# Performance work log

Measured on AMD Instinct MI355X. Metric: run time of the kernel, lower is better.

Reference implementation:

```python
import jax, jax.numpy as jnp
import numpy as np

N = 8192
F_IN = 512
H = 512
E = 128
ALPHA = 0.2
NEG = -9e15


def _xavier(key, shape, gain=1.414):
    fan_in, fan_out = shape[0], shape[1]
    bound = gain * np.sqrt(6.0 / (fan_in + fan_out))
    return jax.random.uniform(key, shape, jnp.float32, -bound, bound)


def setup_inputs() -> dict:
    key = jax.random.key(0)
    ks = jax.random.split(key, 9)
    x = jax.random.normal(ks[0], (N, F_IN), jnp.float32)
    u = jax.random.uniform(ks[1], (N, N), jnp.float32)
    adj = jnp.where(u < 0.05, u, 0.0)
    M = jax.random.uniform(ks[2], (N, N), jnp.float32)
    return {
        "x": x, "adj": adj, "M": M,
        "W1": _xavier(ks[3], (F_IN, H)),
        "a_self1": _xavier(ks[4], (H, 1)),
        "a_neigh1": _xavier(ks[5], (H, 1)),
        "W2": _xavier(ks[6], (H, E)),
        "a_self2": _xavier(ks[7], (E, 1)),
        "a_neigh2": _xavier(ks[8], (E, 1)),
    }


def _gat_layer(x, adj, M, W, a_self, a_neigh):
    h = x @ W                                   # (N, out)
    s = h @ a_self                              # (N, 1)
    n = h @ a_neigh                             # (N, 1)
    e = (s + n.T) * M                           # (N, N) broadcast score sum
    e = jnp.where(e > 0, e, ALPHA * e)          # leaky_relu
    masked = jnp.where(adj > 0, e, NEG)
    attn = jax.nn.softmax(masked, axis=1)
    h_prime = attn @ h
    return jax.nn.elu(h_prime)


def reference(x, adj, M, W1, a_self1, a_neigh1, W2, a_self2, a_neigh2):
    h = _gat_layer(x, adj, M, W1, a_self1, a_neigh1)
    h = _gat_layer(h, adj, M, W2, a_self2, a_neigh2)
    z = h / jnp.maximum(jnp.linalg.norm(h, axis=1, keepdims=True), 1e-12)
    A_pred = jax.nn.sigmoid(z @ z.T)
    return (A_pred, z)
```

## Files before the change

kernel.cpp:

```cpp
#include <hip/hip_runtime.h>
#include <math.h>

#define NNODES 8192
#define CAP 1024
#define KSPLIT 4
#define KCHUNK (NNODES / KSPLIT)

typedef __attribute__((ext_vector_type(8))) short bf16x8;
typedef __attribute__((ext_vector_type(4))) float f32x4;
typedef unsigned short ushort_t;

__device__ inline unsigned short f2bf(float x) {
    unsigned u = __builtin_bit_cast(unsigned, x);
    u += 0x7fffu + ((u >> 16) & 1u);
    return (unsigned short)(u >> 16);
}

#define GLOAD_LDS16(g, l)                                                      \
    __builtin_amdgcn_global_load_lds(                                          \
        (const __attribute__((address_space(1))) void*)(g),                    \
        (__attribute__((address_space(3))) void*)(l), 16, 0, 0)

template <int ROWS>
__device__ inline void stage_tile(ushort_t* lds, const ushort_t* g, size_t ld, int tid)
{
#pragma unroll
    for (int c = 0; c < ROWS / 32; ++c) {
        int row = c * 32 + (tid >> 3);
        int lch = (tid & 7) ^ (row & 7);
        GLOAD_LDS16(g + (size_t)row * ld + lch * 8, lds + (size_t)c * 2048 + tid * 8);
    }
}

__device__ inline int swz_off(int row, int kc) {
    return row * 64 + ((kc ^ (row & 7)) * 8);
}

__global__ __launch_bounds__(256) void gemm64(const float* __restrict__ A,
                                              const float* __restrict__ B,
                                              float* __restrict__ C,
                                              int M, int N, int K)
{
    __shared__ float sA[16][68];
    __shared__ float sB[16][68];

    const int tid = threadIdx.x;
    const int tx = tid & 15, ty = tid >> 4;
    const int bm = blockIdx.x * 64, bn = blockIdx.y * 64;

    float acc[4][4] = {};

    for (int k0 = 0; k0 < K; k0 += 16) {
        for (int l = tid; l < 64 * 16; l += 256) {
            int m = l >> 4, k = l & 15;
            sA[k][m] = A[(size_t)(bm + m) * K + k0 + k];
        }
        for (int l = tid; l < 16 * 64; l += 256) {
            int k = l >> 6, n = l & 63;
            sB[k][n] = B[(size_t)(k0 + k) * N + bn + n];
        }
        __syncthreads();
#pragma unroll
        for (int k = 0; k < 16; ++k) {
            float a[4], b[4];
#pragma unroll
            for (int i = 0; i < 4; ++i) a[i] = sA[k][ty * 4 + i];
#pragma unroll
            for (int j = 0; j < 4; ++j) b[j] = sB[k][tx * 4 + j];
#pragma unroll
            for (int i = 0; i < 4; ++i)
#pragma unroll
                for (int j = 0; j < 4; ++j) acc[i][j] += a[i] * b[j];
        }
        __syncthreads();
    }

#pragma unroll
    for (int i = 0; i < 4; ++i) {
        float4 v = make_float4(acc[i][0], acc[i][1], acc[i][2], acc[i][3]);
        *(float4*)&C[(size_t)(bm + ty * 4 + i) * N + bn + tx * 4] = v;
    }
}

template <int D>
__global__ __launch_bounds__(256) void sn_kernel(const float* __restrict__ h,
                                                 const float* __restrict__ a_s,
                                                 const float* __restrict__ a_n,
                                                 float* __restrict__ sv,
                                                 float* __restrict__ nv)
{
    const int row = (blockIdx.x * 256 + threadIdx.x) >> 6;
    const int lane = threadIdx.x & 63;
    if (row >= NNODES) return;
    const float* hr = h + (size_t)row * D;
    float a0 = 0.f, a1 = 0.f;
#pragma unroll
    for (int k = lane; k < D; k += 64) {
        float hv = hr[k];
        a0 += hv * a_s[k];
        a1 += hv * a_n[k];
    }
#pragma unroll
    for (int o = 32; o; o >>= 1) {
        a0 += __shfl_down(a0, o);
        a1 += __shfl_down(a1, o);
    }
    if (lane == 0) { sv[row] = a0; nv[row] = a1; }
}

__global__ __launch_bounds__(256) void build_csr(const float* __restrict__ adj,
                                                 const float* __restrict__ Mm,
                                                 unsigned short* __restrict__ cols,
                                                 float* __restrict__ vals,
                                                 int* __restrict__ nnzs)
{
    __shared__ __align__(16) float sadj[4][4][256];
    __shared__ __align__(16) float smv[4][4][256];
    __shared__ unsigned short lcol[4][CAP];
    __shared__ float lval[4][CAP];

    const int tid = threadIdx.x;
    const int wid = tid >> 6, lane = tid & 63;
    const int row = blockIdx.x * 4 + wid;
    const float* arow = adj + (size_t)row * NNODES;
    const float* mrow = Mm + (size_t)row * NNODES;
    const size_t base = (size_t)row * CAP;
    const unsigned long long below = (1ull << lane) - 1ull;

    float* sa = &sadj[wid][0][0];
    float* sm = &smv[wid][0][0];
    unsigned short* sc = lcol[wid];
    float* svl = lval[wid];

    int off = 0;

#define ISSUE(t)                                                               \
    do {                                                                       \
        int _s = (t) & 3;                                                      \
        GLOAD_LDS16(arow + (t) * 256 + lane * 4, sa + _s * 256 + lane * 4);    \
        GLOAD_LDS16(mrow + (t) * 256 + lane * 4, sm + _s * 256 + lane * 4);    \
    } while (0)

#define PROCESS(t)                                                             \
    do {                                                                       \
        int _s = (t) & 3;                                                      \
        float4 a = *(const float4*)(sa + _s * 256 + lane * 4);                 \
        float4 mv = *(const float4*)(sm + _s * 256 + lane * 4);                \
        _Pragma("unroll")                                                      \
        for (int e = 0; e < 4; ++e) {                                          \
            float ae = (&a.x)[e];                                              \
            unsigned long long mask = __ballot(ae > 0.f);                      \
            if (ae > 0.f) {                                                    \
                int pos = off + __popcll(mask & below);                        \
                if (pos < CAP) {                                               \
                    sc[pos] = (unsigned short)((t) * 256 + lane * 4 + e);      \
                    svl[pos] = (&mv.x)[e];                                     \
                }                                                              \
            }                                                                  \
            off += __popcll(mask);                                             \
        }                                                                      \
    } while (0)

    ISSUE(0); ISSUE(1); ISSUE(2); ISSUE(3);

    for (int t = 0; t < 28; ++t) {
        asm volatile("s_waitcnt vmcnt(6)" ::: "memory");
        __builtin_amdgcn_sched_barrier(0);
        PROCESS(t);
        ISSUE(t + 4);
    }
    asm volatile("s_waitcnt vmcnt(6)" ::: "memory");
    __builtin_amdgcn_sched_barrier(0);
    PROCESS(28);
    asm volatile("s_waitcnt vmcnt(4)" ::: "memory");
    __builtin_amdgcn_sched_barrier(0);
    PROCESS(29);
    asm volatile("s_waitcnt vmcnt(2)" ::: "memory");
    __builtin_amdgcn_sched_barrier(0);
    PROCESS(30);
    asm volatile("s_waitcnt vmcnt(0)" ::: "memory");
    __builtin_amdgcn_sched_barrier(0);
    PROCESS(31);

#undef ISSUE
#undef PROCESS

    const int nnz = min(off, CAP);
    for (int k = lane; k < nnz; k += 64) {
        cols[base + k] = sc[k];
        vals[base + k] = svl[k];
    }
    if (lane == 0) nnzs[row] = off;
}

__global__ __launch_bounds__(256) void softmax_dense(const unsigned short* __restrict__ cols,
                                                     const float* __restrict__ vals,
                                                     const int* __restrict__ nnzs,
                                                     const float* __restrict__ sv,
                                                     const float* __restrict__ nv,
                                                     ushort_t* __restrict__ P)
{
    constexpr int NT = 256;
    __shared__ ushort_t drow[NNODES];
    __shared__ unsigned short scol[CAP];
    __shared__ float sp[CAP];
    __shared__ float reds[4];
    __shared__ float fb;

    const int tid = threadIdx.x;
    const int i = blockIdx.x;
    const int nnz = min(nnzs[i], CAP);
    const float si = sv[i];
    const size_t base = (size_t)i * CAP;

#pragma unroll
    for (int k = 0; k < NNODES / 8 / NT; ++k)
        ((uint4*)drow)[k * NT + tid] = (uint4){0u, 0u, 0u, 0u};

    float lmax = -3.0e38f;
    for (int k = tid; k < nnz; k += NT) {
        unsigned short c = cols[base + k];
        float e = (si + nv[c]) * vals[base + k];
        e = e > 0.f ? e : 0.2f * e;
        scol[k] = c;
        sp[k] = e;
        lmax = fmaxf(lmax, e);
    }
#pragma unroll
    for (int o = 32; o; o >>= 1) lmax = fmaxf(lmax, __shfl_down(lmax, o));
    if ((tid & 63) == 0) reds[tid >> 6] = lmax;
    __syncthreads();
    if (tid == 0) fb = fmaxf(fmaxf(reds[0], reds[1]), fmaxf(reds[2], reds[3]));
    __syncthreads();
    const float m = fb;

    float lsum = 0.f;
    for (int k = tid; k < nnz; k += NT) {
        float p = expf(sp[k] - m);
        sp[k] = p;
        lsum += p;
    }
#pragma unroll
    for (int o = 32; o; o >>= 1) lsum += __shfl_down(lsum, o);
    if ((tid & 63) == 0) reds[tid >> 6] = lsum;
    __syncthreads();
    if (tid == 0) fb = reds[0] + reds[1] + reds[2] + reds[3];
    __syncthreads();
    const float inv = 1.0f / fb;

    for (int k = tid; k < nnz; k += NT)
        drow[scol[k]] = f2bf(sp[k] * inv);
    __syncthreads();

    uint4* dst = (uint4*)(P + (size_t)i * NNODES);
#pragma unroll
    for (int k = 0; k < NNODES / 8 / NT; ++k)
        dst[k * NT + tid] = ((const uint4*)drow)[k * NT + tid];
}

__global__ __launch_bounds__(256) void tcast(const float* __restrict__ in,
                                             ushort_t* __restrict__ out,
                                             int R, int C)
{
    __shared__ ushort_t t[64][66];
    const int bi = blockIdx.x;
    const int bj = blockIdx.y;
    const int c = threadIdx.x & 63, r4 = threadIdx.x >> 6;
#pragma unroll
    for (int i = 0; i < 16; ++i) {
        int r = i * 4 + r4;
        t[r][c] = f2bf(in[(size_t)(bi * 64 + r) * C + bj * 64 + c]);
    }
    __syncthreads();
#pragma unroll
    for (int i = 0; i < 16; ++i) {
        int r = i * 4 + r4;
        out[(size_t)(bj * 64 + r) * R + bi * 64 + c] = t[c][r];
    }
}

__global__ __launch_bounds__(256) void cast_bf(const float* __restrict__ in,
                                               ushort_t* __restrict__ out, int n4)
{
    int i = blockIdx.x * 256 + threadIdx.x;
    if (i >= n4) return;
    float4 v = ((const float4*)in)[i];
    ushort_t o[4] = { f2bf(v.x), f2bf(v.y), f2bf(v.z), f2bf(v.w) };
    *(uint2*)&out[(size_t)i * 4] = *(uint2*)o;
}

template <int ELU>
__global__ __launch_bounds__(256) void gemm_mfma(const ushort_t* __restrict__ A,
                                                 const ushort_t* __restrict__ BT,
                                                 float* __restrict__ C,
                                                 int N, int K)
{
    __shared__ __align__(16) ushort_t At[128 * 64];
    __shared__ __align__(16) ushort_t Bt[128 * 64];

    const int tid = threadIdx.x;
    const int wid = tid >> 6, lane = tid & 63;
    const int wr = wid >> 1, wc = wid & 1;
    const int bm = blockIdx.x * 128;
    const int bn = blockIdx.y * 128;

    f32x4 acc[4][4] = {};

    for (int k0 = 0; k0 < K; k0 += 64) {
        stage_tile<128>(At, A + (size_t)bm * K + k0, K, tid);
        stage_tile<128>(Bt, BT + (size_t)bn * K + k0, K, tid);
        __syncthreads();
#pragma unroll
        for (int kk = 0; kk < 2; ++kk) {
            const int kc = kk * 4 + (lane >> 4);
            bf16x8 af[4], bfr[4];
#pragma unroll
            for (int m = 0; m < 4; ++m) {
                int r = wr * 64 + m * 16 + (lane & 15);
                af[m] = *(const bf16x8*)&At[swz_off(r, kc)];
            }
#pragma unroll
            for (int n = 0; n < 4; ++n) {
                int r = wc * 64 + n * 16 + (lane & 15);
                bfr[n] = *(const bf16x8*)&Bt[swz_off(r, kc)];
            }
#pragma unroll
            for (int m = 0; m < 4; ++m)
#pragma unroll
                for (int n = 0; n < 4; ++n)
                    acc[m][n] = __builtin_amdgcn_mfma_f32_16x16x32_bf16(af[m], bfr[n], acc[m][n], 0, 0, 0);
        }
        __syncthreads();
    }

#pragma unroll
    for (int m = 0; m < 4; ++m)
#pragma unroll
        for (int n = 0; n < 4; ++n)
#pragma unroll
            for (int r_ = 0; r_ < 4; ++r_) {
                int row = bm + wr * 64 + m * 16 + (lane >> 4) * 4 + r_;
                int col = bn + wc * 64 + n * 16 + (lane & 15);
                float v = acc[m][n][r_];
                if (ELU) v = v > 0.f ? v : expm1f(v);
                C[(size_t)row * N + col] = v;
            }
}

__global__ __launch_bounds__(256) void gemm_pv_ksplit(const ushort_t* __restrict__ P,
                                                      const ushort_t* __restrict__ hbT,
                                                      float* __restrict__ part)
{
    __shared__ __align__(16) ushort_t At[128 * 64];
    __shared__ __align__(16) ushort_t Bt[128 * 64];

    const int tid = threadIdx.x;
    const int wid = tid >> 6, lane = tid & 63;
    const int wr = wid >> 1, wc = wid & 1;
    const int bm = blockIdx.x * 128;
    const int bn = blockIdx.y * 128;
    const int kz = blockIdx.z;

    f32x4 acc[4][4] = {};

    const int kbeg = kz * KCHUNK, kend = kbeg + KCHUNK;
    for (int k0 = kbeg; k0 < kend; k0 += 64) {
        stage_tile<128>(At, P + (size_t)bm * NNODES + k0, NNODES, tid);
        stage_tile<128>(Bt, hbT + (size_t)bn * NNODES + k0, NNODES, tid);
        __syncthreads();
#pragma unroll
        for (int kk = 0; kk < 2; ++kk) {
            const int kc = kk * 4 + (lane >> 4);
            bf16x8 af[4], bfr[4];
#pragma unroll
            for (int m = 0; m < 4; ++m) {
                int r = wr * 64 + m * 16 + (lane & 15);
                af[m] = *(const bf16x8*)&At[swz_off(r, kc)];
            }
#pragma unroll
            for (int n = 0; n < 4; ++n) {
                int r = wc * 64 + n * 16 + (lane & 15);
                bfr[n] = *(const bf16x8*)&Bt[swz_off(r, kc)];
            }
#pragma unroll
            for (int m = 0; m < 4; ++m)
#pragma unroll
                for (int n = 0; n < 4; ++n)
                    acc[m][n] = __builtin_amdgcn_mfma_f32_16x16x32_bf16(af[m], bfr[n], acc[m][n], 0, 0, 0);
        }
        __syncthreads();
    }

    float* dst = part + (size_t)kz * NNODES * 512;
#pragma unroll
    for (int m = 0; m < 4; ++m)
#pragma unroll
        for (int n = 0; n < 4; ++n)
#pragma unroll
            for (int r_ = 0; r_ < 4; ++r_) {
                int row = bm + wr * 64 + m * 16 + (lane >> 4) * 4 + r_;
                int col = bn + wc * 64 + n * 16 + (lane & 15);
                dst[(size_t)row * 512 + col] = acc[m][n][r_];
            }
}

__global__ __launch_bounds__(256) void reduce_elu(const float* __restrict__ part,
                                                  float* __restrict__ out)
{
    const size_t S = (size_t)NNODES * 512 / 4;
    size_t i = (size_t)blockIdx.x * 256 + threadIdx.x;
    if (i >= S) return;
    const float4* p = (const float4*)part;
    float4 a = p[i], b = p[i + S], c = p[i + 2 * S], d = p[i + 3 * S];
    float4 r;
    r.x = a.x + b.x + c.x + d.x;
    r.y = a.y + b.y + c.y + d.y;
    r.z = a.z + b.z + c.z + d.z;
    r.w = a.w + b.w + c.w + d.w;
    r.x = r.x > 0.f ? r.x : expm1f(r.x);
    r.y = r.y > 0.f ? r.y : expm1f(r.y);
    r.z = r.z > 0.f ? r.z : expm1f(r.z);
    r.w = r.w > 0.f ? r.w : expm1f(r.w);
    ((float4*)out)[i] = r;
}

__global__ __launch_bounds__(256) void apred_mfma(const ushort_t* __restrict__ zb,
                                                  float* __restrict__ out)
{
    __shared__ __align__(16) ushort_t At[128 * 64];
    __shared__ __align__(16) ushort_t Bt[128 * 64];

    const int tid = threadIdx.x;
    const int wid = tid >> 6, lane = tid & 63;
    const int wr = wid >> 1, wc = wid & 1;
    const int bm = blockIdx.x * 128;
    const int bn = blockIdx.y * 128;

    f32x4 acc[4][4] = {};

#pragma unroll
    for (int k0 = 0; k0 < 128; k0 += 64) {
        stage_tile<128>(At, zb + (size_t)bm * 128 + k0, 128, tid);
        stage_tile<128>(Bt, zb + (size_t)bn * 128 + k0, 128, tid);
        __syncthreads();
#pragma unroll
        for (int kk = 0; kk < 2; ++kk) {
            const int kc = kk * 4 + (lane >> 4);
            bf16x8 af[4], bfr[4];
#pragma unroll
            for (int m = 0; m < 4; ++m) {
                int r = wr * 64 + m * 16 + (lane & 15);
                af[m] = *(const bf16x8*)&At[swz_off(r, kc)];
            }
#pragma unroll
            for (int n = 0; n < 4; ++n) {
                int r = wc * 64 + n * 16 + (lane & 15);
                bfr[n] = *(const bf16x8*)&Bt[swz_off(r, kc)];
            }
#pragma unroll
            for (int m = 0; m < 4; ++m)
#pragma unroll
                for (int n = 0; n < 4; ++n)
                    acc[m][n] = __builtin_amdgcn_mfma_f32_16x16x32_bf16(af[m], bfr[n], acc[m][n], 0, 0, 0);
        }
        __syncthreads();
    }

#pragma unroll
    for (int m = 0; m < 4; ++m)
#pragma unroll
        for (int n = 0; n < 4; ++n)
#pragma unroll
            for (int r_ = 0; r_ < 4; ++r_) {
                int row = bm + wr * 64 + m * 16 + (lane >> 4) * 4 + r_;
                int col = bn + wc * 64 + n * 16 + (lane & 15);
                float v = acc[m][n][r_];
                out[(size_t)row * NNODES + col] = 1.0f / (1.0f + expf(-v));
            }
}

__global__ __launch_bounds__(256) void attn2_csr(const unsigned short* __restrict__ cols,
                                                 const float* __restrict__ vals,
                                                 const int* __restrict__ nnzs,
                                                 const float* __restrict__ sv,
                                                 const float* __restrict__ nv,
                                                 const ushort_t* __restrict__ h2b,
                                                 float* __restrict__ out)
{
    constexpr int NT = 256;
    __shared__ unsigned short scol[CAP];
    __shared__ float sp[CAP];
    __shared__ float reds[4];
    __shared__ float fb;
    __shared__ float2 part[NT];

    const int tid = threadIdx.x;
    const int i = blockIdx.x;
    const int nnz = min(nnzs[i], CAP);
    const float si = sv[i];
    const size_t base = (size_t)i * CAP;

    float lmax = -3.0e38f;
    for (int k = tid; k < nnz; k += NT) {
        unsigned short c = cols[base + k];
        float e = (si + nv[c]) * vals[base + k];
        e = e > 0.f ? e : 0.2f * e;
        scol[k] = c;
        sp[k] = e;
        lmax = fmaxf(lmax, e);
    }
#pragma unroll
    for (int o = 32; o; o >>= 1) lmax = fmaxf(lmax, __shfl_down(lmax, o));
    if ((tid & 63) == 0) reds[tid >> 6] = lmax;
    __syncthreads();
    if (tid == 0) fb = fmaxf(fmaxf(reds[0], reds[1]), fmaxf(reds[2], reds[3]));
    __syncthreads();
    const float m = fb;

    float lsum = 0.f;
    for (int k = tid; k < nnz; k += NT) {
        float p = expf(sp[k] - m);
        sp[k] = p;
        lsum += p;
    }
#pragma unroll
    for (int o = 32; o; o >>= 1) lsum += __shfl_down(lsum, o);
    if ((tid & 63) == 0) reds[tid >> 6] = lsum;
    __syncthreads();
    if (tid == 0) fb = reds[0] + reds[1] + reds[2] + reds[3];
    __syncthreads();
    const float inv = 1.0f / fb;

    const int g = tid >> 6, lane = tid & 63;
    float ax = 0.f, ay = 0.f;
    for (int k = g; k < nnz; k += 4) {
        float pj = sp[k];
        unsigned hv = *(const unsigned*)&h2b[(size_t)scol[k] * 128 + lane * 2];
        ax += pj * __builtin_bit_cast(float, hv << 16);
        ay += pj * __builtin_bit_cast(float, hv & 0xffff0000u);
    }
    part[tid] = make_float2(ax, ay);
    __syncthreads();
    if (tid < 64) {
        float2 r0 = part[tid], r1 = part[tid + 64], r2 = part[tid + 128], r3 = part[tid + 192];
        float vx = (r0.x + r1.x + r2.x + r3.x) * inv;
        float vy = (r0.y + r1.y + r2.y + r3.y) * inv;
        out[(size_t)i * 128 + tid * 2]     = vx > 0.f ? vx : expm1f(vx);
        out[(size_t)i * 128 + tid * 2 + 1] = vy > 0.f ? vy : expm1f(vy);
    }
}

__global__ __launch_bounds__(256) void norm_kernel(const float* __restrict__ h,
                                                   float* __restrict__ z,
                                                   ushort_t* __restrict__ zb)
{
    const int row = (blockIdx.x * 256 + threadIdx.x) >> 6;
    const int lane = threadIdx.x & 63;
    if (row >= NNODES) return;
    const float* hr = h + (size_t)row * 128;
    float v0 = hr[lane], v1 = hr[lane + 64];
    float ss = v0 * v0 + v1 * v1;
#pragma unroll
    for (int o = 32; o; o >>= 1) ss += __shfl_down(ss, o);
    ss = __shfl(ss, 0);
    float invn = 1.0f / fmaxf(sqrtf(ss), 1e-12f);
    float z0 = v0 * invn, z1 = v1 * invn;
    z[(size_t)row * 128 + lane]      = z0;
    z[(size_t)row * 128 + lane + 64] = z1;
    zb[(size_t)row * 128 + lane]      = f2bf(z0);
    zb[(size_t)row * 128 + lane + 64] = f2bf(z1);
}

template <int D>
__global__ __launch_bounds__(256) void attn_kernel(const float* __restrict__ adj,
                                                   const float* __restrict__ Mm,
                                                   const float* __restrict__ sv,
                                                   const float* __restrict__ nv,
                                                   const float* __restrict__ h,
                                                   float* __restrict__ out)
{
    constexpr int NT = 256;
    constexpr int DCAP = 2048;
    __shared__ float pbuf[NNODES];
    __shared__ int   idxb[DCAP];
    __shared__ int   cnts[NT];
    __shared__ float reds[4];
    __shared__ float fbcast;
    __shared__ int   totc;

    const int tid = threadIdx.x;
    const int i = blockIdx.x;
    const size_t rowoff = (size_t)i * NNODES;
    const float si = sv[i];

    float lmax = -3.0e38f;
    for (int j = tid; j < NNODES; j += NT) {
        float a = adj[rowoff + j];
        float val = -9.0e15f;
        if (a > 0.f) {
            float e = (si + nv[j]) * Mm[rowoff + j];
            val = e > 0.f ? e : 0.2f * e;
            lmax = fmaxf(lmax, val);
        }
        pbuf[j] = val;
    }
#pragma unroll
    for (int o = 32; o; o >>= 1) lmax = fmaxf(lmax, __shfl_down(lmax, o));
    if ((tid & 63) == 0) reds[tid >> 6] = lmax;
    __syncthreads();
    if (tid == 0) fbcast = fmaxf(fmaxf(reds[0], reds[1]), fmaxf(reds[2], reds[3]));
    __syncthreads();
    const float m = fbcast;

    float lsum = 0.f;
    int myc = 0;
    for (int j = tid; j < NNODES; j += NT) {
        float v = pbuf[j];
        float p = (v > -8.9e15f) ? expf(v - m) : 0.f;
        pbuf[j] = p;
        lsum += p;
        if (p > 0.f) myc++;
    }
#pragma unroll
    for (int o = 32; o; o >>= 1) lsum += __shfl_down(lsum, o);
    if ((tid & 63) == 0) reds[tid >> 6] = lsum;
    cnts[tid] = myc;
    __syncthreads();
    if (tid == 0) {
        fbcast = reds[0] + reds[1] + reds[2] + reds[3];
        int run = 0;
        for (int t = 0; t < NT; ++t) { int c = cnts[t]; cnts[t] = run; run += c; }
        totc = run;
    }
    __syncthreads();
    const float inv = 1.0f / fbcast;
    const int nnz = totc;

    if (nnz <= DCAP) {
        int off = cnts[tid];
        for (int j = tid; j < NNODES; j += NT)
            if (pbuf[j] > 0.f) idxb[off++] = j;
    }
    __syncthreads();

    if constexpr (D == 512) {
        const int c = tid;
        float acc0 = 0.f, acc1 = 0.f;
        if (nnz <= DCAP) {
#pragma unroll 4
            for (int t = 0; t < nnz; ++t) {
                int j = idxb[t];
                float pj = pbuf[j];
                const float* hr = h + (size_t)j * 512;
                acc0 += pj * hr[c];
                acc1 += pj * hr[c + 256];
            }
        } else {
            for (int j = 0; j < NNODES; ++j) {
                float pj = pbuf[j];
                if (pj > 0.f) {
                    const float* hr = h + (size_t)j * 512;
                    acc0 += pj * hr[c];
                    acc1 += pj * hr[c + 256];
                }
            }
        }
        float r0 = acc0 * inv, r1 = acc1 * inv;
        out[(size_t)i * 512 + c]       = r0 > 0.f ? r0 : expm1f(r0);
        out[(size_t)i * 512 + c + 256] = r1 > 0.f ? r1 : expm1f(r1);
    } else {
        const int half = tid >> 7;
        const int c = tid & 127;
        float acc = 0.f;
        if (nnz <= DCAP) {
#pragma unroll 4
            for (int t = half; t < nnz; t += 2) {
                int j = idxb[t];
                acc += pbuf[j] * h[(size_t)j * 128 + c];
            }
        } else {
            for (int j = half; j < NNODES; j += 2) {
                float pj = pbuf[j];
                if (pj > 0.f) acc += pj * h[(size_t)j * 128 + c];
            }
        }
        __syncthreads();
        pbuf[tid] = acc;
        __syncthreads();
        if (tid < 128) {
            float r = (pbuf[tid] + pbuf[tid + 128]) * inv;
            out[(size_t)i * 128 + tid] = r > 0.f ? r : expm1f(r);
        }
    }
}

__global__ __launch_bounds__(256) void apred_kernel(const float* __restrict__ z,
                                                    float* __restrict__ out)
{
    __shared__ float sA[32][68];
    __shared__ float sB[32][68];

    const int tid = threadIdx.x;
    const int tx = tid & 15, ty = tid >> 4;
    const int bm = blockIdx.x * 64, bn = blockIdx.y * 64;

    float acc[4][4] = {};

    for (int k0 = 0; k0 < 128; k0 += 32) {
        for (int l = tid; l < 64 * 32; l += 256) {
            int r = l >> 5, kk = l & 31;
            sA[kk][r] = z[(size_t)(bm + r) * 128 + k0 + kk];
            sB[kk][r] = z[(size_t)(bn + r) * 128 + k0 + kk];
        }
        __syncthreads();
#pragma unroll
        for (int kk = 0; kk < 32; ++kk) {
            float a[4], b[4];
#pragma unroll
            for (int i = 0; i < 4; ++i) a[i] = sA[kk][ty * 4 + i];
#pragma unroll
            for (int j = 0; j < 4; ++j) b[j] = sB[kk][tx * 4 + j];
#pragma unroll
            for (int i = 0; i < 4; ++i)
#pragma unroll
                for (int j = 0; j < 4; ++j) acc[i][j] += a[i] * b[j];
        }
        __syncthreads();
    }

#pragma unroll
    for (int i = 0; i < 4; ++i) {
        float4 v;
        v.x = 1.0f / (1.0f + expf(-acc[i][0]));
        v.y = 1.0f / (1.0f + expf(-acc[i][1]));
        v.z = 1.0f / (1.0f + expf(-acc[i][2]));
        v.w = 1.0f / (1.0f + expf(-acc[i][3]));
        *(float4*)&out[(size_t)(bm + ty * 4 + i) * NNODES + bn + tx * 4] = v;
    }
}

extern "C" void kernel_launch(void* const* d_in, const int* in_sizes, int n_in,
                              void* d_out, int out_size, void* d_ws, size_t ws_size,
                              hipStream_t stream)
{
    const float* x   = (const float*)d_in[0];
    const float* adj = (const float*)d_in[1];
    const float* Mm  = (const float*)d_in[2];
    const float* W1  = (const float*)d_in[3];
    const float* as1 = (const float*)d_in[4];
    const float* an1 = (const float*)d_in[5];
    const float* W2  = (const float*)d_in[6];
    const float* as2 = (const float*)d_in[7];
    const float* an2 = (const float*)d_in[8];

    float* out   = (float*)d_out;
    float* Apred = out;
    float* z     = out + (size_t)NNODES * NNODES;

    ushort_t* P    = (ushort_t*)Apred;
    ushort_t* hbT  = (ushort_t*)((char*)Apred + (size_t)134217728);
    float*    part = (float*)((char*)Apred + (size_t)142606336);

    float* ws  = (float*)d_ws;
    float* h1  = ws;
    float* h1p = h1 + (size_t)NNODES * 512;
    float* h2p = h1p + (size_t)NNODES * 512;
    float* sv  = h2p + (size_t)NNODES * 128;
    float* nv  = sv + NNODES;
    float* vals = nv + NNODES;
    unsigned short* cols = (unsigned short*)(vals + (size_t)NNODES * CAP);
    int* nnzs = (int*)(cols + (size_t)NNODES * CAP);
    ushort_t* zb  = (ushort_t*)(nnzs + NNODES);
    ushort_t* h2b = zb + (size_t)NNODES * 128;
    ushort_t* xb  = h2b + (size_t)NNODES * 128;
    ushort_t* W1T = xb + (size_t)NNODES * 512;

    const size_t need = (size_t)((char*)(W1T + 512 * 512) - (char*)d_ws);

    if (ws_size >= need) {
        cast_bf<<<dim3(4096), 256, 0, stream>>>(x, xb, NNODES * 512 / 4);
        tcast<<<dim3(8, 8), 256, 0, stream>>>(W1, W1T, 512, 512);
        gemm_mfma<0><<<dim3(64, 4), 256, 0, stream>>>(xb, W1T, h1, 512, 512);
        sn_kernel<512><<<dim3(2048), 256, 0, stream>>>(h1, as1, an1, sv, nv);

        build_csr<<<dim3(2048), 256, 0, stream>>>(adj, Mm, cols, vals, nnzs);
        softmax_dense<<<dim3(NNODES), 256, 0, stream>>>(cols, vals, nnzs, sv, nv, P);

        tcast<<<dim3(128, 8), 256, 0, stream>>>(h1, hbT, NNODES, 512);
        gemm_pv_ksplit<<<dim3(64, 4, KSPLIT), 256, 0, stream>>>(P, hbT, part);
        reduce_elu<<<dim3(NNODES * 512 / 4 / 256), 256, 0, stream>>>(part, h1p);

        gemm64<<<dim3(128, 2), 256, 0, stream>>>(h1p, W2, h1, NNODES, 128, 512);
        sn_kernel<128><<<dim3(2048), 256, 0, stream>>>(h1, as2, an2, sv, nv);
        cast_bf<<<dim3(1024), 256, 0, stream>>>(h1, h2b, NNODES * 128 / 4);
        attn2_csr<<<dim3(NNODES), 256, 0, stream>>>(cols, vals, nnzs, sv, nv, h2b, h2p);

        norm_kernel<<<dim3(2048), 256, 0, stream>>>(h2p, z, zb);
        apred_mfma<<<dim3(64, 64), 256, 0, stream>>>(zb, Apred);
    } else {
        gemm64<<<dim3(128, 8), 256, 0, stream>>>(x, W1, h1, NNODES, 512, 512);
        sn_kernel<512><<<dim3(2048), 256, 0, stream>>>(h1, as1, an1, sv, nv);
        attn_kernel<512><<<dim3(NNODES), 256, 0, stream>>>(adj, Mm, sv, nv, h1, h1p);

        gemm64<<<dim3(128, 2), 256, 0, stream>>>(h1p, W2, h1, NNODES, 128, 512);
        sn_kernel<128><<<dim3(2048), 256, 0, stream>>>(h1, as2, an2, sv, nv);
        attn_kernel<128><<<dim3(NNODES), 256, 0, stream>>>(adj, Mm, sv, nv, h1, h2p);

        norm_kernel<<<dim3(2048), 256, 0, stream>>>(h2p, z, zb);
        apred_kernel<<<dim3(128, 128), 256, 0, stream>>>(z, Apred);
    }
}
```

Baseline: 584.2 us.

## Split CSR build to gather M sparsely and stage A_pred stores through LDS

```diff
diff --git a/kernel.cpp b/kernel.cpp
--- a/kernel.cpp
+++ b/kernel.cpp
@@ -108,89 +108,45 @@
     if (lane == 0) { sv[row] = a0; nv[row] = a1; }
 }
 
-__global__ __launch_bounds__(256) void build_csr(const float* __restrict__ adj,
-                                                 const float* __restrict__ Mm,
-                                                 unsigned short* __restrict__ cols,
-                                                 float* __restrict__ vals,
-                                                 int* __restrict__ nnzs)
-{
-    __shared__ __align__(16) float sadj[4][4][256];
-    __shared__ __align__(16) float smv[4][4][256];
-    __shared__ unsigned short lcol[4][CAP];
-    __shared__ float lval[4][CAP];
-
-    const int tid = threadIdx.x;
-    const int wid = tid >> 6, lane = tid & 63;
-    const int row = blockIdx.x * 4 + wid;
-    const float* arow = adj + (size_t)row * NNODES;
-    const float* mrow = Mm + (size_t)row * NNODES;
+__global__ __launch_bounds__(256) void build_cols(const float* __restrict__ adj,
+                                                  unsigned short* __restrict__ cols,
+                                                  int* __restrict__ nnzs)
+{
+    const int lane = threadIdx.x & 63;
+    const int row = blockIdx.x * 4 + (threadIdx.x >> 6);
+    const float4* arow = (const float4*)(adj + (size_t)row * NNODES);
     const size_t base = (size_t)row * CAP;
     const unsigned long long below = (1ull << lane) - 1ull;
 
-    float* sa = &sadj[wid][0][0];
-    float* sm = &smv[wid][0][0];
-    unsigned short* sc = lcol[wid];
-    float* svl = lval[wid];
-
     int off = 0;
-
-#define ISSUE(t)                                                               \
-    do {                                                                       \
-        int _s = (t) & 3;                                                      \
-        GLOAD_LDS16(arow + (t) * 256 + lane * 4, sa + _s * 256 + lane * 4);    \
-        GLOAD_LDS16(mrow + (t) * 256 + lane * 4, sm + _s * 256 + lane * 4);    \
-    } while (0)
-
-#define PROCESS(t)                                                             \
-    do {                                                                       \
-        int _s = (t) & 3;                                                      \
-        float4 a = *(const float4*)(sa + _s * 256 + lane * 4);                 \
-        float4 mv = *(const float4*)(sm + _s * 256 + lane * 4);                \
-        _Pragma("unroll")                                                      \
-        for (int e = 0; e < 4; ++e) {                                          \
-            float ae = (&a.x)[e];                                              \
-            unsigned long long mask = __ballot(ae > 0.f);                      \
-            if (ae > 0.f) {                                                    \
-                int pos = off + __popcll(mask & below);                        \
-                if (pos < CAP) {                                               \
-                    sc[pos] = (unsigned short)((t) * 256 + lane * 4 + e);      \
-                    svl[pos] = (&mv.x)[e];                                     \
-                }                                                              \
-            }                                                                  \
-            off += __popcll(mask);                                             \
-        }                                                                      \
-    } while (0)
-
-    ISSUE(0); ISSUE(1); ISSUE(2); ISSUE(3);
-
-    for (int t = 0; t < 28; ++t) {
-        asm volatile("s_waitcnt vmcnt(6)" ::: "memory");
-        __builtin_amdgcn_sched_barrier(0);
-        PROCESS(t);
-        ISSUE(t + 4);
-    }
-    asm volatile("s_waitcnt vmcnt(6)" ::: "memory");
-    __builtin_amdgcn_sched_barrier(0);
-    PROCESS(28);
-    asm volatile("s_waitcnt vmcnt(4)" ::: "memory");
-    __builtin_amdgcn_sched_barrier(0);
-    PROCESS(29);
-    asm volatile("s_waitcnt vmcnt(2)" ::: "memory");
-    __builtin_amdgcn_sched_barrier(0);
-    PROCESS(30);
-    asm volatile("s_waitcnt vmcnt(0)" ::: "memory");
-    __builtin_amdgcn_sched_barrier(0);
-    PROCESS(31);
-
-#undef ISSUE
-#undef PROCESS
-
-    const int nnz = min(off, CAP);
-    for (int k = lane; k < nnz; k += 64) {
-        cols[base + k] = sc[k];
-        vals[base + k] = svl[k];
+    for (int c4 = 0; c4 < NNODES / 4; c4 += 64) {
+        float4 a = arow[c4 + lane];
+#pragma unroll
+        for (int e = 0; e < 4; ++e) {
+            float ae = (&a.x)[e];
+            unsigned long long mask = __ballot(ae > 0.f);
+            if (ae > 0.f) {
+                int pos = off + __popcll(mask & below);
+                if (pos < CAP)
+                    cols[base + pos] = (unsigned short)((c4 + lane) * 4 + e);
+            }
+            off += __popcll(mask);
+        }
     }
     if (lane == 0) nnzs[row] = off;
+}
+
+__global__ __launch_bounds__(256) void gather_vals(const unsigned short* __restrict__ cols,
+                                                   const float* __restrict__ Mm,
+                                                   const int* __restrict__ nnzs,
+                                                   float* __restrict__ vals)
+{
+    const int i = blockIdx.x;
+    const int nnz = min(nnzs[i], CAP);
+    const size_t base = (size_t)i * CAP;
+    const size_t rowoff = (size_t)i * NNODES;
+    for (int k = threadIdx.x; k < nnz; k += 256)
+        vals[base + k] = Mm[rowoff + cols[base + k]];
 }
 
 __global__ __launch_bounds__(256) void softmax_dense(const unsigned short* __restrict__ cols,
@@ -427,8 +383,9 @@
 __global__ __launch_bounds__(256) void apred_mfma(const ushort_t* __restrict__ zb,
                                                   float* __restrict__ out)
 {
-    __shared__ __align__(16) ushort_t At[128 * 64];
-    __shared__ __align__(16) ushort_t Bt[128 * 64];
+    __shared__ __align__(16) char smem[4 * 64 * 68 * 4];
+    ushort_t* At = (ushort_t*)smem;
+    ushort_t* Bt = (ushort_t*)(smem + 16384);
 
     const int tid = threadIdx.x;
     const int wid = tid >> 6, lane = tid & 63;
@@ -466,17 +423,28 @@
         __syncthreads();
     }
 
+    float* cb = (float*)smem + (size_t)wid * 64 * 68;
 #pragma unroll
     for (int m = 0; m < 4; ++m)
 #pragma unroll
         for (int n = 0; n < 4; ++n)
 #pragma unroll
             for (int r_ = 0; r_ < 4; ++r_) {
-                int row = bm + wr * 64 + m * 16 + (lane >> 4) * 4 + r_;
-                int col = bn + wc * 64 + n * 16 + (lane & 15);
+                int rl = m * 16 + (lane >> 4) * 4 + r_;
+                int cl = n * 16 + (lane & 15);
                 float v = acc[m][n][r_];
-                out[(size_t)row * NNODES + col] = 1.0f / (1.0f + expf(-v));
-            }
+                cb[rl * 68 + cl] = 1.0f / (1.0f + expf(-v));
+            }
+
+    const int rowbase = bm + wr * 64;
+    const int colbase = bn + wc * 64;
+#pragma unroll
+    for (int j = 0; j < 16; ++j) {
+        int rl = j * 4 + (lane >> 4);
+        int c4 = (lane & 15) * 4;
+        float4 v = *(const float4*)&cb[rl * 68 + c4];
+        *(float4*)&out[(size_t)(rowbase + rl) * NNODES + colbase + c4] = v;
+    }
 }
 
 __global__ __launch_bounds__(256) void attn2_csr(const unsigned short* __restrict__ cols,
@@ -783,7 +751,8 @@
         gemm_mfma<0><<<dim3(64, 4), 256, 0, stream>>>(xb, W1T, h1, 512, 512);
         sn_kernel<512><<<dim3(2048), 256, 0, stream>>>(h1, as1, an1, sv, nv);
 
-        build_csr<<<dim3(2048), 256, 0, stream>>>(adj, Mm, cols, vals, nnzs);
+        build_cols<<<dim3(2048), 256, 0, stream>>>(adj, cols, nnzs);
+        gather_vals<<<dim3(NNODES), 256, 0, stream>>>(cols, Mm, nnzs, vals);
         softmax_dense<<<dim3(NNODES), 256, 0, stream>>>(cols, vals, nnzs, sv, nv, P);
 
         tcast<<<dim3(128, 8), 256, 0, stream>>>(h1, hbT, NNODES, 512);
```

Result: faster. 564.1 us (-3.4%).
